# Performance work log

Hardware: AMD Instinct MI355X
Metric: run time of the kernel (lower is better)

Reference implementation:

```python
import jax, jax.numpy as jnp
import numpy as np

B, L, D = 4, 2048, 512
H, DK, DV = 8, 64, 64


def setup_inputs() -> dict:
    key = jax.random.key(0)
    ks = jax.random.split(key, 12)
    s = 0.02
    return {
        "query": jax.random.normal(ks[0], (B, L, D), jnp.float32),
        "key": jax.random.normal(ks[1], (B, L, D), jnp.float32),
        "value": jax.random.normal(ks[2], (B, L, D), jnp.float32),
        "attention_mask": jax.random.normal(ks[3], (1, 1, L, L), jnp.float32),
        "Wq": jax.random.normal(ks[4], (D, H * DK), jnp.float32) * s,
        "bq": jnp.zeros((H * DK,), jnp.float32),
        "Wk": jax.random.normal(ks[5], (D, H * DK), jnp.float32) * s,
        "bk": jnp.zeros((H * DK,), jnp.float32),
        "Wv": jax.random.normal(ks[6], (D, H * DV), jnp.float32) * s,
        "bv": jnp.zeros((H * DV,), jnp.float32),
        "Wo": jax.random.normal(ks[7], (H * DV, D), jnp.float32) * s,
        "bo": jnp.zeros((D,), jnp.float32),
    }


def reference(query, key, value, attention_mask, Wq, bq, Wk, bk, Wv, bv, Wo, bo):
    sz_b, len_q, _ = query.shape
    len_k = key.shape[1]
    # projections -> [B, L, H, d]
    q = (query @ Wq + bq).reshape(sz_b, len_q, H, DK)
    k = (key @ Wk + bk).reshape(sz_b, len_k, H, DK)
    v = (value @ Wv + bv).reshape(sz_b, len_k, H, DV)
    # permute(2,0,1,3): heads first -> [H, B, L, d]
    q = jnp.transpose(q, (2, 0, 1, 3))
    k = jnp.transpose(k, (2, 0, 1, 3))
    v = jnp.transpose(v, (2, 0, 1, 3))
    scale = 1.0 / jnp.sqrt(jnp.asarray(DK, q.dtype))
    scores = jnp.einsum('hbqd,hbkd->hbqk', q, k) * scale + attention_mask
    attn = jax.nn.softmax(scores, axis=-1)
    x = jnp.einsum('hbqk,hbkd->hbqd', attn, v)  # [H, B, Lq, Dv]
    # faithful to torch: transpose(1,2) -> [H, Lq, B, Dv] then view(B, Lq, H*Dv)
    x = jnp.transpose(x, (0, 2, 1, 3)).reshape(sz_b, len_q, H * DV)
    return x @ Wo + bo
```

## Files before the change

### kernel.cpp

```cpp
#include <hip/hip_runtime.h>

#define SEQ    2048
#define DMODEL 512
#define NHEAD  8
#define HDIM   64
#define BATCH  4
#define NROWS  65536
#define KSPLIT 2

#define LOG2E  1.4426950408889634f
#define QSCALE 0.18033688011112042f

typedef float f32x4  __attribute__((ext_vector_type(4)));
typedef float f32x16 __attribute__((ext_vector_type(16)));
typedef _Float16 h16x8 __attribute__((ext_vector_type(8)));
typedef _Float16 h16x2 __attribute__((ext_vector_type(2)));

union U4H { uint4 u; h16x8 h; };
union U1H2 { unsigned int u; h16x2 h; };

static __device__ inline h16x2 pkrtz(float a, float b) {
    return __builtin_bit_cast(h16x2, __builtin_amdgcn_cvt_pkrtz(a, b));
}
static __device__ inline unsigned short f2h(float x) {
    _Float16 h = (_Float16)x;
    return __builtin_bit_cast(unsigned short, h);
}
static __device__ inline void async_cp16(const void* g, void* l) {
    __builtin_amdgcn_global_load_lds(
        (const __attribute__((address_space(1))) unsigned int*)g,
        (__attribute__((address_space(3))) unsigned int*)l,
        16, 0, 0);
}

__global__ __launch_bounds__(256) void transpose_cast_w(
    const float* __restrict__ s0, const float* __restrict__ s1,
    const float* __restrict__ s2, const float* __restrict__ s3,
    unsigned short* __restrict__ d0, unsigned short* __restrict__ d1,
    unsigned short* __restrict__ d2, unsigned short* __restrict__ d3)
{
    const float* S; unsigned short* D;
    switch (blockIdx.z) {
        case 0: S = s0; D = d0; break;
        case 1: S = s1; D = d1; break;
        case 2: S = s2; D = d2; break;
        default: S = s3; D = d3; break;
    }
    __shared__ float T[32][33];
    const int t = threadIdx.x;
    const int r = t >> 3, c = (t & 7) * 4;
    const int k0 = blockIdx.x * 32, n0 = blockIdx.y * 32;
    float4 v = *(const float4*)&S[(size_t)(k0 + r) * DMODEL + n0 + c];
    T[r][c] = v.x; T[r][c + 1] = v.y; T[r][c + 2] = v.z; T[r][c + 3] = v.w;
    __syncthreads();
    ushort4 o;
    o.x = f2h(T[c + 0][r]); o.y = f2h(T[c + 1][r]);
    o.z = f2h(T[c + 2][r]); o.w = f2h(T[c + 3][r]);
    *(ushort4*)&D[(size_t)(n0 + r) * DMODEL + k0 + c] = o;
}

__global__ __launch_bounds__(256) void prep_mask(
    const float* __restrict__ mask, unsigned short* __restrict__ mp)
{
    int i = blockIdx.x * 256 + threadIdx.x;
    int k = (i * 4) & (SEQ - 1);
    int q = (i * 4) >> 11;
    float4 v = ((const float4*)mask)[i];
    int kt = k >> 6, kl = k & 63;
    int mt = kl >> 5, g = (kl >> 3) & 3, hl = (kl >> 2) & 1;
    size_t base = ((size_t)kt * SEQ + q) * 64 + hl * 32 + mt * 16 + g * 4;
    ushort4 o;
    o.x = f2h(__builtin_amdgcn_exp2f(v.x * LOG2E));
    o.y = f2h(__builtin_amdgcn_exp2f(v.y * LOG2E));
    o.z = f2h(__builtin_amdgcn_exp2f(v.z * LOG2E));
    o.w = f2h(__builtin_amdgcn_exp2f(v.w * LOG2E));
    *(ushort4*)&mp[base] = o;
}

template <int A_FP32, int EPI>
static __device__ inline void gemm_core(
    const void* __restrict__ Ap, const unsigned short* __restrict__ Bt,
    const float* __restrict__ bias, void* __restrict__ Cout, float oscale,
    int bm, int bn)
{
    __shared__ __align__(16) unsigned short As[128 * 32];
    __shared__ __align__(16) unsigned short Bs[128 * 32];

    const int t = threadIdx.x;
    const int lane = t & 63, w = t >> 6;
    const int wm = w >> 1, wn = w & 1;
    const int c = lane & 15, quad = lane >> 4;

    f32x4 acc[4][4] = {};

    for (int k0 = 0; k0 < DMODEL; k0 += 32) {
        if (A_FP32) {
            const float* Af = (const float*)Ap;
            #pragma unroll
            for (int p = 0; p < 4; p++) {
                int cid = p * 256 + t;
                int row = cid >> 3, fc = cid & 7;
                float4 av = *(const float4*)&Af[(size_t)(bm + row) * DMODEL + k0 + fc * 4];
                U1H2 lo, hi;
                lo.h = pkrtz(av.x, av.y);
                hi.h = pkrtz(av.z, av.w);
                uint2 st = make_uint2(lo.u, hi.u);
                *(uint2*)&As[row * 32 + fc * 4] = st;
            }
        } else {
            const unsigned short* Ab = (const unsigned short*)Ap;
            #pragma unroll
            for (int i = 0; i < 2; i++) {
                int row = 32 * w + 16 * i + (lane >> 2);
                const unsigned short* gp = Ab + (size_t)(bm + row) * DMODEL + k0 + (lane & 3) * 8;
                async_cp16(gp, &As[(32 * w + 16 * i) * 32]);
            }
        }
        #pragma unroll
        for (int i = 0; i < 2; i++) {
            int row = 32 * w + 16 * i + (lane >> 2);
            const unsigned short* gp = Bt + (size_t)(bn + row) * DMODEL + k0 + (lane & 3) * 8;
            async_cp16(gp, &Bs[(32 * w + 16 * i) * 32]);
        }
        __syncthreads();

        U4H af[4], bf[4];
        #pragma unroll
        for (int mt = 0; mt < 4; mt++)
            af[mt].u = *(const uint4*)&As[(wm * 64 + mt * 16 + c) * 32 + quad * 8];
        #pragma unroll
        for (int nt = 0; nt < 4; nt++)
            bf[nt].u = *(const uint4*)&Bs[(wn * 64 + nt * 16 + c) * 32 + quad * 8];
        #pragma unroll
        for (int mt = 0; mt < 4; mt++)
            #pragma unroll
            for (int nt = 0; nt < 4; nt++)
                acc[mt][nt] = __builtin_amdgcn_mfma_f32_16x16x32_f16(
                    af[mt].h, bf[nt].h, acc[mt][nt], 0, 0, 0);
        __syncthreads();
    }

    if (EPI == 2) {
        #pragma unroll
        for (int nt = 0; nt < 4; nt++) {
            int ng = bn + wn * 64 + nt * 16 + c;
            int h = ng >> 6, dv = ng & 63;
            float bv = bias[ng];
            #pragma unroll
            for (int mt = 0; mt < 4; mt++) {
                int mg0 = bm + wm * 64 + mt * 16 + quad * 4;
                int bb = mg0 >> 11, key0 = mg0 & (SEQ - 1);
                U1H2 lo, hi;
                lo.h = pkrtz(acc[mt][nt][0] + bv, acc[mt][nt][1] + bv);
                hi.h = pkrtz(acc[mt][nt][2] + bv, acc[mt][nt][3] + bv);
                *(uint2*)&((unsigned short*)Cout)[
                    ((size_t)(bb * NHEAD + h) * HDIM + dv) * SEQ + key0] =
                    make_uint2(lo.u, hi.u);
            }
        }
        return;
    }
    #pragma unroll
    for (int nt = 0; nt < 4; nt++) {
        int ng = bn + wn * 64 + nt * 16 + c;
        float bv = bias[ng];
        #pragma unroll
        for (int mt = 0; mt < 4; mt++) {
            #pragma unroll
            for (int r = 0; r < 4; r++) {
                int mg = bm + wm * 64 + mt * 16 + quad * 4 + r;
                float v = (acc[mt][nt][r] + bv) * oscale;
                if (EPI == 1)
                    ((unsigned short*)Cout)[(size_t)mg * DMODEL + ng] = f2h(v);
                else
                    ((float*)Cout)[(size_t)mg * DMODEL + ng] = v;
            }
        }
    }
}

struct QKVArgs {
    const float *A0, *A1, *A2;
    const unsigned short *W0, *W1, *W2;
    const float *b0, *b1, *b2;
    unsigned short *o0, *o1, *o2;
};

__global__ __launch_bounds__(256) void gemm_qkv(QKVArgs a) {
    if (blockIdx.z == 2)
        gemm_core<1, 2>(a.A2, a.W2, a.b2, a.o2, 1.0f, blockIdx.y * 128, blockIdx.x * 128);
    else if (blockIdx.z == 1)
        gemm_core<1, 1>(a.A1, a.W1, a.b1, a.o1, 1.0f, blockIdx.y * 128, blockIdx.x * 128);
    else
        gemm_core<1, 1>(a.A0, a.W0, a.b0, a.o0, QSCALE, blockIdx.y * 128, blockIdx.x * 128);
}

__global__ __launch_bounds__(256) void gemm_fin(
    const unsigned short* __restrict__ A, const unsigned short* __restrict__ W,
    const float* __restrict__ bias, float* __restrict__ C) {
    gemm_core<0, 0>(A, W, bias, C, 1.0f, blockIdx.y * 128, blockIdx.x * 128);
}

__global__ __launch_bounds__(256, 3) void attn5(
    const unsigned short* __restrict__ qb, const unsigned short* __restrict__ kb,
    const unsigned short* __restrict__ vT, const unsigned short* __restrict__ emp,
    unsigned short* __restrict__ Xp, float* __restrict__ Lp)
{
    __shared__ __align__(16) unsigned short Ks[2][64 * 64];
    __shared__ __align__(16) unsigned short Vs[2][64 * 64];

    const int t = threadIdx.x;
    const int lane = t & 63, w = t >> 6;
    const int c32 = lane & 31, hl = lane >> 5;
    const int bh = blockIdx.x, b = bh >> 3, head = bh & 7;
    const int q0 = blockIdx.y * 128;
    const int split = blockIdx.z;
    const int qg = q0 + w * 32 + c32;

    const unsigned short* qrow = qb + ((size_t)b * SEQ + qg) * DMODEL + head * HDIM;
    U4H Qf[4];
    #pragma unroll
    for (int s = 0; s < 4; s++)
        Qf[s].u = *(const uint4*)&qrow[s * 16 + hl * 8];

    const unsigned short* kgb = kb + (size_t)b * SEQ * DMODEL + head * HDIM
                              + (size_t)split * 1024 * DMODEL;
    const unsigned short* vgb = vT + (size_t)bh * HDIM * SEQ + split * 1024;

    const int srow = lane >> 3;
    const int sch  = (lane & 7) ^ srow;

    {
        #pragma unroll
        for (int i = 0; i < 2; i++) {
            int row = w * 16 + i * 8 + srow;
            async_cp16(&kgb[(size_t)row * DMODEL + sch * 8], &Ks[0][(w * 16 + i * 8) * 64]);
            async_cp16(&vgb[(size_t)row * SEQ + sch * 8],    &Vs[0][(w * 16 + i * 8) * 64]);
        }
    }

    f32x16 O0 = {}, O1 = {};
    float lsum = 0.f;

    for (int kt = 0; kt < 1024 / 64; kt++) {
        const int p = kt & 1;
        __syncthreads();

        const int ktg = split * 16 + kt;
        const unsigned short* mrow = emp + ((size_t)ktg * SEQ + qg) * 64 + hl * 32;
        U4H e0, e1, e2, e3;
        e0.u = *(const uint4*)&mrow[0];
        e1.u = *(const uint4*)&mrow[8];
        e2.u = *(const uint4*)&mrow[16];
        e3.u = *(const uint4*)&mrow[24];

        if (kt + 1 < 1024 / 64) {
            int k0n = (kt + 1) * 64;
            #pragma unroll
            for (int i = 0; i < 2; i++) {
                int row = w * 16 + i * 8 + srow;
                async_cp16(&kgb[(size_t)(k0n + row) * DMODEL + sch * 8],
                           &Ks[p ^ 1][(w * 16 + i * 8) * 64]);
                async_cp16(&vgb[(size_t)row * SEQ + k0n + sch * 8],
                           &Vs[p ^ 1][(w * 16 + i * 8) * 64]);
            }
        }

        const unsigned short* Kp = Ks[p];
        const unsigned short* Vp = Vs[p];

        f32x16 S0 = {}, S1 = {};
        #pragma unroll
        for (int s = 0; s < 4; s++) {
            int fc = 2 * s + hl;
            int sl = (fc ^ (c32 & 7)) * 8;
            U4H ka0, ka1;
            ka0.u = *(const uint4*)&Kp[c32 * 64 + sl];
            ka1.u = *(const uint4*)&Kp[(32 + c32) * 64 + sl];
            S0 = __builtin_amdgcn_mfma_f32_32x32x16_f16(ka0.h, Qf[s].h, S0, 0, 0, 0);
            S1 = __builtin_amdgcn_mfma_f32_32x32x16_f16(ka1.h, Qf[s].h, S1, 0, 0, 0);
        }

        unsigned int Pf[4][4];
        #pragma unroll
        for (int mt = 0; mt < 2; mt++) {
            f32x16 S = mt ? S1 : S0;
            h16x8 ea = (mt ? e2 : e0).h;
            h16x8 eb = (mt ? e3 : e1).h;
            unsigned int u[4][2];
            #pragma unroll
            for (int jj = 0; jj < 8; jj++) {
                _Float16 exl = (jj < 4) ? ea[2 * jj]     : eb[2 * jj - 8];
                _Float16 exh = (jj < 4) ? ea[2 * jj + 1] : eb[2 * jj - 7];
                h16x2 ex = {exl, exh};
                h16x2 pk = pkrtz(__builtin_amdgcn_exp2f(S[2 * jj]),
                                 __builtin_amdgcn_exp2f(S[2 * jj + 1]));
                h16x2 pp = pk * ex;
                lsum += (float)pp[0] + (float)pp[1];
                u[jj >> 1][jj & 1] = __builtin_bit_cast(unsigned int, pp);
            }
            unsigned int sA0 = hl ? u[0][0] : u[1][0];
            unsigned int sA1 = hl ? u[0][1] : u[1][1];
            unsigned int sB0 = hl ? u[2][0] : u[3][0];
            unsigned int sB1 = hl ? u[2][1] : u[3][1];
            unsigned int rA0 = (unsigned)__shfl_xor((int)sA0, 32, 64);
            unsigned int rA1 = (unsigned)__shfl_xor((int)sA1, 32, 64);
            unsigned int rB0 = (unsigned)__shfl_xor((int)sB0, 32, 64);
            unsigned int rB1 = (unsigned)__shfl_xor((int)sB1, 32, 64);
            Pf[2 * mt + 0][0] = hl ? rA0 : u[0][0];
            Pf[2 * mt + 0][1] = hl ? rA1 : u[0][1];
            Pf[2 * mt + 0][2] = hl ? u[1][0] : rA0;
            Pf[2 * mt + 0][3] = hl ? u[1][1] : rA1;
            Pf[2 * mt + 1][0] = hl ? rB0 : u[2][0];
            Pf[2 * mt + 1][1] = hl ? rB1 : u[2][1];
            Pf[2 * mt + 1][2] = hl ? u[3][0] : rB0;
            Pf[2 * mt + 1][3] = hl ? u[3][1] : rB1;
        }

        #pragma unroll
        for (int s = 0; s < 4; s++) {
            int kc = 2 * s + hl;
            int sl = (kc ^ (c32 & 7)) * 8;
            U4H va0, va1, pu;
            va0.u = *(const uint4*)&Vp[c32 * 64 + sl];
            va1.u = *(const uint4*)&Vp[(32 + c32) * 64 + sl];
            pu.u = make_uint4(Pf[s][0], Pf[s][1], Pf[s][2], Pf[s][3]);
            O0 = __builtin_amdgcn_mfma_f32_32x32x16_f16(va0.h, pu.h, O0, 0, 0, 0);
            O1 = __builtin_amdgcn_mfma_f32_32x32x16_f16(va1.h, pu.h, O1, 0, 0, 0);
        }
    }

    lsum += __shfl_xor(lsum, 32, 64);
    const size_t j = ((size_t)head * SEQ + qg) * BATCH + b;
    unsigned short* xr = Xp + ((size_t)split * NROWS + j) * HDIM;
    #pragma unroll
    for (int mt = 0; mt < 2; mt++) {
        f32x16 Ov = mt ? O1 : O0;
        #pragma unroll
        for (int g = 0; g < 4; g++) {
            U1H2 lo, hi;
            lo.h = pkrtz(Ov[g * 4 + 0], Ov[g * 4 + 1]);
            hi.h = pkrtz(Ov[g * 4 + 2], Ov[g * 4 + 3]);
            uint2 st = make_uint2(lo.u, hi.u);
            *(uint2*)&xr[mt * 32 + 8 * g + 4 * hl] = st;
        }
    }
    if (hl == 0) Lp[split * NROWS + j] = lsum;
}

__global__ __launch_bounds__(256) void combine_attn(
    const unsigned short* __restrict__ Xp, const float* __restrict__ Lp,
    unsigned short* __restrict__ xb)
{
    int i = blockIdx.x * 256 + threadIdx.x;
    int j = i >> 3, dc = (i & 7) * 8;
    U4H a, b;
    a.u = *(const uint4*)&Xp[(size_t)j * HDIM + dc];
    b.u = *(const uint4*)&Xp[((size_t)NROWS + j) * HDIM + dc];
    float inv = 1.0f / (Lp[j] + Lp[NROWS + j]);
    U4H o;
    #pragma unroll
    for (int p = 0; p < 4; p++) {
        float s0 = ((float)a.h[2 * p]     + (float)b.h[2 * p])     * inv;
        float s1 = ((float)a.h[2 * p + 1] + (float)b.h[2 * p + 1]) * inv;
        h16x2 pk = pkrtz(s0, s1);
        o.h[2 * p] = pk[0]; o.h[2 * p + 1] = pk[1];
    }
    *(uint4*)&xb[(size_t)j * HDIM + dc] = o.u;
}

extern "C" void kernel_launch(void* const* d_in, const int* in_sizes, int n_in,
                              void* d_out, int out_size, void* d_ws, size_t ws_size,
                              hipStream_t stream) {
    const float* query = (const float*)d_in[0];
    const float* key_  = (const float*)d_in[1];
    const float* value = (const float*)d_in[2];
    const float* mask  = (const float*)d_in[3];
    const float* Wq = (const float*)d_in[4];
    const float* bq = (const float*)d_in[5];
    const float* Wk = (const float*)d_in[6];
    const float* bk = (const float*)d_in[7];
    const float* Wv = (const float*)d_in[8];
    const float* bv = (const float*)d_in[9];
    const float* Wo = (const float*)d_in[10];
    const float* bo = (const float*)d_in[11];
    float* out = (float*)d_out;

    const size_t NP = (size_t)BATCH * SEQ * DMODEL;
    unsigned short* ws   = (unsigned short*)d_ws;
    unsigned short* qb16 = ws;
    unsigned short* kb16 = qb16 + NP;
    unsigned short* vT16 = kb16 + NP;
    unsigned short* xb16 = vT16 + NP;
    unsigned short* em16 = xb16 + NP;
    unsigned short* Xp16 = em16 + (size_t)SEQ * SEQ;
    unsigned short* WqT  = Xp16 + (size_t)KSPLIT * NROWS * HDIM;
    unsigned short* WkT  = WqT + DMODEL * DMODEL;
    unsigned short* WvT  = WkT + DMODEL * DMODEL;
    unsigned short* WoT  = WvT + DMODEL * DMODEL;
    float* Lp = (float*)(WoT + DMODEL * DMODEL);

    transpose_cast_w<<<dim3(16, 16, 4), 256, 0, stream>>>(
        Wq, Wk, Wv, Wo, WqT, WkT, WvT, WoT);
    prep_mask<<<dim3(SEQ * SEQ / 4 / 256), 256, 0, stream>>>(mask, em16);

    QKVArgs qa;
    qa.A0 = query; qa.A1 = key_; qa.A2 = value;
    qa.W0 = WqT;   qa.W1 = WkT;  qa.W2 = WvT;
    qa.b0 = bq;    qa.b1 = bk;   qa.b2 = bv;
    qa.o0 = qb16;  qa.o1 = kb16; qa.o2 = vT16;
    gemm_qkv<<<dim3(DMODEL / 128, BATCH * SEQ / 128, 3), 256, 0, stream>>>(qa);

    attn5<<<dim3(BATCH * NHEAD, SEQ / 128, KSPLIT), 256, 0, stream>>>(
        qb16, kb16, vT16, em16, Xp16, Lp);

    combine_attn<<<dim3(NROWS * 8 / 256), 256, 0, stream>>>(Xp16, Lp, xb16);

    gemm_fin<<<dim3(DMODEL / 128, BATCH * SEQ / 128), 256, 0, stream>>>(
        xb16, WoT, bo, out);
}
```

Before: 253.2 us.

## Pre-cast inputs to fp16, double-buffer GEMM LDS, and tune attention inner loop

Adds a separate kernel that casts query/key/value to fp16 so the QKV GEMM can use async global-to-LDS copies. The GEMM gains double-buffered, XOR-swizzled LDS tiles that prefetch the next K slice during compute. The attention loop prefetches the next mask tile, raises wave priority around MFMA blocks, uses fdot2 for the row sum and permlane32_swap instead of shuffles. The extra cast pass adds memory traffic and reuses scratch buffers.

```diff
diff --git a/kernel.cpp b/kernel.cpp
--- a/kernel.cpp
+++ b/kernel.cpp
@@ -15,6 +15,7 @@
 typedef float f32x16 __attribute__((ext_vector_type(16)));
 typedef _Float16 h16x8 __attribute__((ext_vector_type(8)));
 typedef _Float16 h16x2 __attribute__((ext_vector_type(2)));
+typedef unsigned int u32x2 __attribute__((ext_vector_type(2)));
 
 union U4H { uint4 u; h16x8 h; };
 union U1H2 { unsigned int u; h16x2 h; };
@@ -77,60 +78,76 @@
     *(ushort4*)&mp[base] = o;
 }
 
-template <int A_FP32, int EPI>
-static __device__ inline void gemm_core(
-    const void* __restrict__ Ap, const unsigned short* __restrict__ Bt,
+__global__ __launch_bounds__(256) void cast_a16(
+    const float* __restrict__ s0, const float* __restrict__ s1,
+    const float* __restrict__ s2,
+    unsigned short* __restrict__ d0, unsigned short* __restrict__ d1,
+    unsigned short* __restrict__ d2)
+{
+    const float* S; unsigned short* D;
+    switch (blockIdx.z) {
+        case 0: S = s0; D = d0; break;
+        case 1: S = s1; D = d1; break;
+        default: S = s2; D = d2; break;
+    }
+    size_t i = ((size_t)blockIdx.x * 256 + threadIdx.x) * 8;
+    float4 a = *(const float4*)&S[i];
+    float4 b = *(const float4*)&S[i + 4];
+    U1H2 p0, p1, p2, p3;
+    p0.h = pkrtz(a.x, a.y); p1.h = pkrtz(a.z, a.w);
+    p2.h = pkrtz(b.x, b.y); p3.h = pkrtz(b.z, b.w);
+    *(uint4*)&D[i] = make_uint4(p0.u, p1.u, p2.u, p3.u);
+}
+
+template <int EPI>
+static __device__ inline void gemm_core16(
+    const unsigned short* __restrict__ Ab, const unsigned short* __restrict__ Bt,
     const float* __restrict__ bias, void* __restrict__ Cout, float oscale,
     int bm, int bn)
 {
-    __shared__ __align__(16) unsigned short As[128 * 32];
-    __shared__ __align__(16) unsigned short Bs[128 * 32];
+    __shared__ __align__(16) unsigned short As[2][128 * 32];
+    __shared__ __align__(16) unsigned short Bs[2][128 * 32];
 
     const int t = threadIdx.x;
     const int lane = t & 63, w = t >> 6;
     const int wm = w >> 1, wn = w & 1;
     const int c = lane & 15, quad = lane >> 4;
+    const int srow = lane >> 2;
+    const int sck  = (lane & 3) ^ ((lane >> 3) & 3);
 
     f32x4 acc[4][4] = {};
 
+    #pragma unroll
+    for (int i = 0; i < 2; i++) {
+        int row = 32 * w + 16 * i + srow;
+        async_cp16(Ab + (size_t)(bm + row) * DMODEL + sck * 8,
+                   &As[0][(32 * w + 16 * i) * 32]);
+        async_cp16(Bt + (size_t)(bn + row) * DMODEL + sck * 8,
+                   &Bs[0][(32 * w + 16 * i) * 32]);
+    }
+    __syncthreads();
+
+    const int slot8 = (quad ^ ((c >> 1) & 3)) * 8;
+
     for (int k0 = 0; k0 < DMODEL; k0 += 32) {
-        if (A_FP32) {
-            const float* Af = (const float*)Ap;
-            #pragma unroll
-            for (int p = 0; p < 4; p++) {
-                int cid = p * 256 + t;
-                int row = cid >> 3, fc = cid & 7;
-                float4 av = *(const float4*)&Af[(size_t)(bm + row) * DMODEL + k0 + fc * 4];
-                U1H2 lo, hi;
-                lo.h = pkrtz(av.x, av.y);
-                hi.h = pkrtz(av.z, av.w);
-                uint2 st = make_uint2(lo.u, hi.u);
-                *(uint2*)&As[row * 32 + fc * 4] = st;
+        const int cur = (k0 >> 5) & 1;
+        if (k0 + 32 < DMODEL) {
+            #pragma unroll
+            for (int i = 0; i < 2; i++) {
+                int row = 32 * w + 16 * i + srow;
+                async_cp16(Ab + (size_t)(bm + row) * DMODEL + k0 + 32 + sck * 8,
+                           &As[cur ^ 1][(32 * w + 16 * i) * 32]);
+                async_cp16(Bt + (size_t)(bn + row) * DMODEL + k0 + 32 + sck * 8,
+                           &Bs[cur ^ 1][(32 * w + 16 * i) * 32]);
             }
-        } else {
-            const unsigned short* Ab = (const unsigned short*)Ap;
-            #pragma unroll
-            for (int i = 0; i < 2; i++) {
-                int row = 32 * w + 16 * i + (lane >> 2);
-                const unsigned short* gp = Ab + (size_t)(bm + row) * DMODEL + k0 + (lane & 3) * 8;
-                async_cp16(gp, &As[(32 * w + 16 * i) * 32]);
-            }
-        }
-        #pragma unroll
-        for (int i = 0; i < 2; i++) {
-            int row = 32 * w + 16 * i + (lane >> 2);
-            const unsigned short* gp = Bt + (size_t)(bn + row) * DMODEL + k0 + (lane & 3) * 8;
-            async_cp16(gp, &Bs[(32 * w + 16 * i) * 32]);
-        }
-        __syncthreads();
-
+        }
         U4H af[4], bf[4];
         #pragma unroll
         for (int mt = 0; mt < 4; mt++)
-            af[mt].u = *(const uint4*)&As[(wm * 64 + mt * 16 + c) * 32 + quad * 8];
+            af[mt].u = *(const uint4*)&As[cur][(wm * 64 + mt * 16 + c) * 32 + slot8];
         #pragma unroll
         for (int nt = 0; nt < 4; nt++)
-            bf[nt].u = *(const uint4*)&Bs[(wn * 64 + nt * 16 + c) * 32 + quad * 8];
+            bf[nt].u = *(const uint4*)&Bs[cur][(wn * 64 + nt * 16 + c) * 32 + slot8];
         #pragma unroll
         for (int mt = 0; mt < 4; mt++)
             #pragma unroll
@@ -180,7 +197,7 @@
 }
 
 struct QKVArgs {
-    const float *A0, *A1, *A2;
+    const unsigned short *A0, *A1, *A2;
     const unsigned short *W0, *W1, *W2;
     const float *b0, *b1, *b2;
     unsigned short *o0, *o1, *o2;
@@ -188,17 +205,17 @@
 
 __global__ __launch_bounds__(256) void gemm_qkv(QKVArgs a) {
     if (blockIdx.z == 2)
-        gemm_core<1, 2>(a.A2, a.W2, a.b2, a.o2, 1.0f, blockIdx.y * 128, blockIdx.x * 128);
+        gemm_core16<2>(a.A2, a.W2, a.b2, a.o2, 1.0f, blockIdx.y * 128, blockIdx.x * 128);
     else if (blockIdx.z == 1)
-        gemm_core<1, 1>(a.A1, a.W1, a.b1, a.o1, 1.0f, blockIdx.y * 128, blockIdx.x * 128);
+        gemm_core16<1>(a.A1, a.W1, a.b1, a.o1, 1.0f, blockIdx.y * 128, blockIdx.x * 128);
     else
-        gemm_core<1, 1>(a.A0, a.W0, a.b0, a.o0, QSCALE, blockIdx.y * 128, blockIdx.x * 128);
+        gemm_core16<1>(a.A0, a.W0, a.b0, a.o0, QSCALE, blockIdx.y * 128, blockIdx.x * 128);
 }
 
 __global__ __launch_bounds__(256) void gemm_fin(
     const unsigned short* __restrict__ A, const unsigned short* __restrict__ W,
     const float* __restrict__ bias, float* __restrict__ C) {
-    gemm_core<0, 0>(A, W, bias, C, 1.0f, blockIdx.y * 128, blockIdx.x * 128);
+    gemm_core16<0>(A, W, bias, C, 1.0f, blockIdx.y * 128, blockIdx.x * 128);
 }
 
 __global__ __launch_bounds__(256, 3) void attn5(
@@ -239,20 +256,22 @@
         }
     }
 
-    f32x16 O0 = {}, O1 = {};
-    float lsum = 0.f;
-
-    for (int kt = 0; kt < 1024 / 64; kt++) {
-        const int p = kt & 1;
-        __syncthreads();
-
-        const int ktg = split * 16 + kt;
-        const unsigned short* mrow = emp + ((size_t)ktg * SEQ + qg) * 64 + hl * 32;
-        U4H e0, e1, e2, e3;
+    U4H e0, e1, e2, e3;
+    {
+        const unsigned short* mrow = emp + ((size_t)(split * 16) * SEQ + qg) * 64 + hl * 32;
         e0.u = *(const uint4*)&mrow[0];
         e1.u = *(const uint4*)&mrow[8];
         e2.u = *(const uint4*)&mrow[16];
         e3.u = *(const uint4*)&mrow[24];
+    }
+
+    f32x16 O0 = {}, O1 = {};
+    float lsum = 0.f;
+    const h16x2 one2 = {(_Float16)1.0f, (_Float16)1.0f};
+
+    for (int kt = 0; kt < 1024 / 64; kt++) {
+        const int p = kt & 1;
+        __syncthreads();
 
         if (kt + 1 < 1024 / 64) {
             int k0n = (kt + 1) * 64;
@@ -266,10 +285,22 @@
             }
         }
 
+        U4H f0, f1, f2, f3;
+        {
+            int ktn = (kt + 1 < 1024 / 64) ? kt + 1 : kt;
+            const unsigned short* mrow =
+                emp + ((size_t)(split * 16 + ktn) * SEQ + qg) * 64 + hl * 32;
+            f0.u = *(const uint4*)&mrow[0];
+            f1.u = *(const uint4*)&mrow[8];
+            f2.u = *(const uint4*)&mrow[16];
+            f3.u = *(const uint4*)&mrow[24];
+        }
+
         const unsigned short* Kp = Ks[p];
         const unsigned short* Vp = Vs[p];
 
         f32x16 S0 = {}, S1 = {};
+        __builtin_amdgcn_s_setprio(1);
         #pragma unroll
         for (int s = 0; s < 4; s++) {
             int fc = 2 * s + hl;
@@ -280,6 +311,7 @@
             S0 = __builtin_amdgcn_mfma_f32_32x32x16_f16(ka0.h, Qf[s].h, S0, 0, 0, 0);
             S1 = __builtin_amdgcn_mfma_f32_32x32x16_f16(ka1.h, Qf[s].h, S1, 0, 0, 0);
         }
+        __builtin_amdgcn_s_setprio(0);
 
         unsigned int Pf[4][4];
         #pragma unroll
@@ -296,9 +328,23 @@
                 h16x2 pk = pkrtz(__builtin_amdgcn_exp2f(S[2 * jj]),
                                  __builtin_amdgcn_exp2f(S[2 * jj + 1]));
                 h16x2 pp = pk * ex;
+#if __has_builtin(__builtin_amdgcn_fdot2)
+                lsum = __builtin_amdgcn_fdot2(pp, one2, lsum, false);
+#else
                 lsum += (float)pp[0] + (float)pp[1];
+#endif
                 u[jj >> 1][jj & 1] = __builtin_bit_cast(unsigned int, pp);
             }
+#if __has_builtin(__builtin_amdgcn_permlane32_swap)
+            u32x2 rA0 = __builtin_amdgcn_permlane32_swap(u[0][0], u[1][0], false, false);
+            u32x2 rA1 = __builtin_amdgcn_permlane32_swap(u[0][1], u[1][1], false, false);
+            u32x2 rB0 = __builtin_amdgcn_permlane32_swap(u[2][0], u[3][0], false, false);
+            u32x2 rB1 = __builtin_amdgcn_permlane32_swap(u[2][1], u[3][1], false, false);
+            Pf[2 * mt + 0][0] = rA0[0]; Pf[2 * mt + 0][1] = rA1[0];
+            Pf[2 * mt + 0][2] = rA0[1]; Pf[2 * mt + 0][3] = rA1[1];
+            Pf[2 * mt + 1][0] = rB0[0]; Pf[2 * mt + 1][1] = rB1[0];
+            Pf[2 * mt + 1][2] = rB0[1]; Pf[2 * mt + 1][3] = rB1[1];
+#else
             unsigned int sA0 = hl ? u[0][0] : u[1][0];
             unsigned int sA1 = hl ? u[0][1] : u[1][1];
             unsigned int sB0 = hl ? u[2][0] : u[3][0];
@@ -315,8 +361,10 @@
             Pf[2 * mt + 1][1] = hl ? rB1 : u[2][1];
             Pf[2 * mt + 1][2] = hl ? u[3][0] : rB0;
             Pf[2 * mt + 1][3] = hl ? u[3][1] : rB1;
-        }
-
+#endif
+        }
+
+        __builtin_amdgcn_s_setprio(1);
         #pragma unroll
         for (int s = 0; s < 4; s++) {
             int kc = 2 * s + hl;
@@ -328,6 +376,9 @@
             O0 = __builtin_amdgcn_mfma_f32_32x32x16_f16(va0.h, pu.h, O0, 0, 0, 0);
             O1 = __builtin_amdgcn_mfma_f32_32x32x16_f16(va1.h, pu.h, O1, 0, 0, 0);
         }
+        __builtin_amdgcn_s_setprio(0);
+
+        e0 = f0; e1 = f1; e2 = f2; e3 = f3;
     }
 
     lsum += __shfl_xor(lsum, 32, 64);
@@ -400,15 +451,21 @@
     unsigned short* WoT  = WvT + DMODEL * DMODEL;
     float* Lp = (float*)(WoT + DMODEL * DMODEL);
 
+    unsigned short* q16 = xb16;
+    unsigned short* k16 = Xp16;
+    unsigned short* v16 = Xp16 + NP;
+
     transpose_cast_w<<<dim3(16, 16, 4), 256, 0, stream>>>(
         Wq, Wk, Wv, Wo, WqT, WkT, WvT, WoT);
     prep_mask<<<dim3(SEQ * SEQ / 4 / 256), 256, 0, stream>>>(mask, em16);
+    cast_a16<<<dim3(NP / 8 / 256, 1, 3), 256, 0, stream>>>(
+        query, key_, value, q16, k16, v16);
 
     QKVArgs qa;
-    qa.A0 = query; qa.A1 = key_; qa.A2 = value;
-    qa.W0 = WqT;   qa.W1 = WkT;  qa.W2 = WvT;
-    qa.b0 = bq;    qa.b1 = bk;   qa.b2 = bv;
-    qa.o0 = qb16;  qa.o1 = kb16; qa.o2 = vT16;
+    qa.A0 = q16;  qa.A1 = k16;  qa.A2 = v16;
+    qa.W0 = WqT;  qa.W1 = WkT;  qa.W2 = WvT;
+    qa.b0 = bq;   qa.b1 = bk;   qa.b2 = bv;
+    qa.o0 = qb16; qa.o1 = kb16; qa.o2 = vT16;
     gemm_qkv<<<dim3(DMODEL / 128, BATCH * SEQ / 128, 3), 256, 0, stream>>>(qa);
 
     attn5<<<dim3(BATCH * NHEAD, SEQ / 128, KSPLIT), 256, 0, stream>>>(
```

After: 235.7 us. -6.9%, faster.
